# Optimization experiments

Hardware: AMD Instinct MI355X
Metric: run time of the kernel (lower is better)

## Reference

```python
import jax, jax.numpy as jnp
import numpy as np

TOP_K = 8
ROUTED_SCALING_FACTOR = 1.0
EPS = 1e-20


def setup_inputs() -> dict:
    key = jax.random.key(0)
    k1, k2, k3 = jax.random.split(key, 3)
    T, D, E = 8192, 4096, 64
    x = jax.random.normal(k1, (T, D), dtype=jnp.float32)
    gate_weight = jax.random.normal(k2, (E, D), dtype=jnp.float32) * (1.0 / np.sqrt(D))
    bias = jax.random.normal(k3, (E,), dtype=jnp.float32) * 0.1
    return {"x": x, "gate_weight": gate_weight, "bias": bias}


def reference(x, gate_weight, bias):
    # logits: [T, E] = x [T, D] @ gate_weight.T [D, E]
    logits = jnp.einsum('td,ed->te', x.astype(jnp.float32), gate_weight)
    scores = jax.nn.sigmoid(logits)
    biased = scores + bias  # broadcast [E]
    # top-k on biased scores, sorted descending
    _, indices = jax.lax.top_k(biased, TOP_K)  # [T, K]
    selected_scores = jnp.take_along_axis(scores, indices, axis=-1)  # [T, K]
    normalized = selected_scores / (jnp.sum(selected_scores, axis=-1, keepdims=True) + EPS)
    weights = normalized * ROUTED_SCALING_FACTOR
    return (indices, weights)
```

## Files before the change

kernel.cpp:

```cpp
#include <hip/hip_runtime.h>
#include <math.h>
#include <stdint.h>

#define T_TOK 8192
#define DDIM  4096
#define NEXP  64
#define TOPK  8
#define MT    128
#define BK    32
#define RS    2048.0f

typedef __attribute__((ext_vector_type(8))) _Float16 half8;
typedef __attribute__((ext_vector_type(4))) float f32x4;
typedef __attribute__((address_space(3))) uint32_t lds_u32;
typedef const __attribute__((address_space(1))) uint32_t glb_u32;

template<int STEPS, int S>
__global__ __launch_bounds__(512) void gemm_part(
    const float* __restrict__ x, const float* __restrict__ gw,
    float* __restrict__ part)
{
    __shared__ float A[2][MT * BK];
    __shared__ float Bf[2][2048];

    const int tid  = threadIdx.x;
    const int lane = tid & 63;
    const int wv   = tid >> 6;
    const int wm   = wv & 3;
    const int wn   = wv >> 2;
    const int slc  = blockIdx.x % S;
    const int mt   = blockIdx.x / S;
    const int m0   = mt * MT;
    const int kt0  = slc * STEPS;
    const int am   = lane & 15;
    const int ag   = lane >> 4;

    const int s_row0 = tid >> 3;
    const int s_c    = tid & 7;

    const int bn = wv & 3;
    const int bh = wv >> 2;
    const float* gB = gw + (size_t)(bn * 16 + am) * DDIM
                    + (size_t)kt0 * BK + ag * 8 + bh * 4;

#define STAGE(buf_, t_) do {                                                   \
        const size_t koff = (size_t)(kt0 + (t_)) * BK;                         \
        int c0 = s_c ^ (s_row0 & 7);                                           \
        __builtin_amdgcn_global_load_lds(                                      \
            (glb_u32*)(x + (size_t)(m0 + s_row0) * DDIM + koff + c0 * 4),      \
            (lds_u32*)(&A[buf_][tid * 4]), 16, 0, 0);                          \
        int r1 = s_row0 + 64;                                                  \
        int c1 = s_c ^ (r1 & 7);                                               \
        __builtin_amdgcn_global_load_lds(                                      \
            (glb_u32*)(x + (size_t)(m0 + r1) * DDIM + koff + c1 * 4),          \
            (lds_u32*)(&A[buf_][2048 + tid * 4]), 16, 0, 0);                   \
        __builtin_amdgcn_global_load_lds(                                      \
            (glb_u32*)(gB + (size_t)(t_) * BK),                                \
            (lds_u32*)(&Bf[buf_][((bn * 2 + bh) * 64 + lane) * 4]), 16, 0, 0); \
    } while (0)

    f32x4 aH[2][2], aM[2][2];
    #pragma unroll
    for (int f = 0; f < 2; f++)
        #pragma unroll
        for (int n = 0; n < 2; n++) {
            aH[f][n] = (f32x4){0.f, 0.f, 0.f, 0.f};
            aM[f][n] = (f32x4){0.f, 0.f, 0.f, 0.f};
        }

    STAGE(0, 0);
    __syncthreads();

    #pragma unroll 2
    for (int t = 0; t < STEPS; t++) {
        const int buf = t & 1;
        if (t + 1 < STEPS) STAGE(buf ^ 1, t + 1);

        half8 B0[2], B1[2];
        #pragma unroll
        for (int nf = 0; nf < 2; nf++) {
            const int n = wn * 2 + nf;
            float4 u0 = *reinterpret_cast<const float4*>(
                &Bf[buf][((n * 2 + 0) * 64 + lane) * 4]);
            float4 u1 = *reinterpret_cast<const float4*>(
                &Bf[buf][((n * 2 + 1) * 64 + lane) * 4]);
            const float bv[8] = {u0.x, u0.y, u0.z, u0.w, u1.x, u1.y, u1.z, u1.w};
            #pragma unroll
            for (int j = 0; j < 8; j++) {
                float v = bv[j];
                _Float16 h = (_Float16)v;
                B0[nf][j] = h;
                B1[nf][j] = (_Float16)((v - (float)h) * RS);
            }
        }

        #pragma unroll
        for (int f = 0; f < 2; f++) {
            const int row = wm * 32 + f * 16 + am;
            const int sw  = am & 7;
            float4 alo = *reinterpret_cast<const float4*>(
                &A[buf][row * BK + ((ag * 2 + 0) ^ sw) * 4]);
            float4 ahi = *reinterpret_cast<const float4*>(
                &A[buf][row * BK + ((ag * 2 + 1) ^ sw) * 4]);
            const float vv[8] = {alo.x, alo.y, alo.z, alo.w,
                                 ahi.x, ahi.y, ahi.z, ahi.w};
            half8 a0, a1;
            #pragma unroll
            for (int j = 0; j < 8; j++) {
                float v = vv[j];
                _Float16 h = (_Float16)v;
                a0[j] = h;
                a1[j] = (_Float16)((v - (float)h) * RS);
            }
            #pragma unroll
            for (int nf = 0; nf < 2; nf++) {
                aH[f][nf] = __builtin_amdgcn_mfma_f32_16x16x32_f16(a0, B0[nf], aH[f][nf], 0, 0, 0);
                aM[f][nf] = __builtin_amdgcn_mfma_f32_16x16x32_f16(a0, B1[nf], aM[f][nf], 0, 0, 0);
                aM[f][nf] = __builtin_amdgcn_mfma_f32_16x16x32_f16(a1, B0[nf], aM[f][nf], 0, 0, 0);
            }
        }
        __syncthreads();
    }
#undef STAGE

    const float i1 = 1.0f / RS;
    float* po = part + (size_t)slc * T_TOK * NEXP + (size_t)m0 * NEXP;
    #pragma unroll
    for (int f = 0; f < 2; f++)
        #pragma unroll
        for (int nf = 0; nf < 2; nf++)
            #pragma unroll
            for (int r = 0; r < 4; r++)
                po[(size_t)(wm * 32 + f * 16 + ag * 4 + r) * NEXP
                   + (wn * 2 + nf) * 16 + am]
                    = aH[f][nf][r] + aM[f][nf][r] * i1;
}

__global__ __launch_bounds__(256) void reduce_topk(
    const float* __restrict__ part, const float* __restrict__ bias,
    float* __restrict__ out, int S)
{
    const int wave = threadIdx.x >> 6;
    const int lane = threadIdx.x & 63;
    const int j    = blockIdx.x;
    const int g    = j & 7;
    const int q    = j >> 3;
    const int token = g * 128 + (q & 31) * 4 + (q >> 5) * 1024 + wave;
    if (token >= T_TOK) return;

    float logit = 0.f;
    for (int s = 0; s < S; s++)
        logit += part[(size_t)s * T_TOK * NEXP + (size_t)token * NEXP + lane];

    float score  = 1.f / (1.f + expf(-logit));
    float biased = score + bias[lane];

    float my_sc = 0.f;
    int   my_idx = 0;
    float ssum  = 0.f;

    #pragma unroll
    for (int jj = 0; jj < TOPK; jj++) {
        float v = biased;
        int   i = lane;
        #pragma unroll
        for (int off = 32; off >= 1; off >>= 1) {
            float ov = __shfl_xor(v, off);
            int   oi = __shfl_xor(i, off);
            if (ov > v || (ov == v && oi < i)) { v = ov; i = oi; }
        }
        float s_sel = __shfl(score, i);
        ssum += s_sel;
        if (lane == jj) { my_idx = i; my_sc = s_sel; }
        if (lane == i) biased = -INFINITY;
    }

    if (lane < TOPK) {
        out[(size_t)token * TOPK + lane] = (float)my_idx;
        out[(size_t)T_TOK * TOPK + (size_t)token * TOPK + lane]
            = my_sc / (ssum + 1e-20f);
    }
}

extern "C" void kernel_launch(void* const* d_in, const int* in_sizes, int n_in,
                              void* d_out, int out_size, void* d_ws, size_t ws_size,
                              hipStream_t stream) {
    (void)in_sizes; (void)n_in; (void)out_size;
    const float* x    = (const float*)d_in[0];
    const float* gw   = (const float*)d_in[1];
    const float* bias = (const float*)d_in[2];
    float* out  = (float*)d_out;
    float* part = (float*)d_ws;

    const size_t per_slice = (size_t)T_TOK * NEXP * sizeof(float);
    int S = 1;
    for (int cand : {8, 4, 2}) {
        if ((size_t)cand * per_slice <= ws_size) { S = cand; break; }
    }

    dim3 b1(512);
    switch (S) {
        case 8: gemm_part<16, 8><<<dim3(64 * 8), b1, 0, stream>>>(x, gw, part); break;
        case 4: gemm_part<32, 4><<<dim3(64 * 4), b1, 0, stream>>>(x, gw, part); break;
        case 2: gemm_part<64, 2><<<dim3(64 * 2), b1, 0, stream>>>(x, gw, part); break;
        default: gemm_part<128, 1><<<dim3(64), b1, 0, stream>>>(x, gw, part); break;
    }

    reduce_topk<<<dim3(T_TOK / 4), 256, 0, stream>>>(part, bias, out, S);
}
```

Measured before the change: 45.90 us.

## Add 256-row M tile GEMM variant with 16-way split-K

Adds a GEMM kernel with 256-token tiles where each of 8 waves covers 32 rows and all 64 experts. Each wave converts the B (gate weight) fragments to split-fp16 once and reuses them across both of its row fragments. The split-K factor also rises to 16 when the workspace allows, keeping 512 blocks. This is meant to cut redundant B loads and conversions per token, but it doubles the partial-sum traffic the reduce kernel must read and adds register pressure from the larger accumulator set.

```diff
diff --git a/kernel.cpp b/kernel.cpp
--- a/kernel.cpp
+++ b/kernel.cpp
@@ -6,7 +6,6 @@
 #define DDIM  4096
 #define NEXP  64
 #define TOPK  8
-#define MT    128
 #define BK    32
 #define RS    2048.0f
 
@@ -16,11 +15,126 @@
 typedef const __attribute__((address_space(1))) uint32_t glb_u32;
 
 template<int STEPS, int S>
-__global__ __launch_bounds__(512) void gemm_part(
+__global__ __launch_bounds__(512, 4) void gemm_part256(
     const float* __restrict__ x, const float* __restrict__ gw,
     float* __restrict__ part)
 {
-    __shared__ float A[2][MT * BK];
+    __shared__ float A[2][256 * BK];
+    __shared__ float Bf[2][2048];
+
+    const int tid  = threadIdx.x;
+    const int lane = tid & 63;
+    const int wv   = tid >> 6;
+    const int slc  = blockIdx.x % S;
+    const int mt   = blockIdx.x / S;
+    const int m0   = mt * 256;
+    const int kt0  = slc * STEPS;
+    const int am   = lane & 15;
+    const int ag   = lane >> 4;
+
+    const int bn = wv & 3;
+    const int bh = wv >> 2;
+    const float* gB = gw + (size_t)(bn * 16 + am) * DDIM
+                    + (size_t)kt0 * BK + ag * 8 + bh * 4;
+
+#define STAGE(buf_, t_) do {                                                   \
+        const size_t koff = (size_t)(kt0 + (t_)) * BK;                         \
+        _Pragma("unroll")                                                      \
+        for (int r_ = 0; r_ < 4; r_++) {                                       \
+            int idx_ = r_ * 512 + tid;                                         \
+            int row_ = idx_ >> 3;                                              \
+            int c_   = idx_ & 7;                                               \
+            int cs_  = c_ ^ (row_ & 7);                                        \
+            __builtin_amdgcn_global_load_lds(                                  \
+                (glb_u32*)(x + (size_t)(m0 + row_) * DDIM + koff + cs_ * 4),   \
+                (lds_u32*)(&A[buf_][idx_ * 4]), 16, 0, 0);                     \
+        }                                                                      \
+        __builtin_amdgcn_global_load_lds(                                      \
+            (glb_u32*)(gB + (size_t)(t_) * BK),                                \
+            (lds_u32*)(&Bf[buf_][((bn * 2 + bh) * 64 + lane) * 4]), 16, 0, 0); \
+    } while (0)
+
+    f32x4 aH[2][4], aM[2][4];
+    #pragma unroll
+    for (int f = 0; f < 2; f++)
+        #pragma unroll
+        for (int n = 0; n < 4; n++) {
+            aH[f][n] = (f32x4){0.f, 0.f, 0.f, 0.f};
+            aM[f][n] = (f32x4){0.f, 0.f, 0.f, 0.f};
+        }
+
+    STAGE(0, 0);
+    __syncthreads();
+
+    for (int t = 0; t < STEPS; t++) {
+        const int buf = t & 1;
+        if (t + 1 < STEPS) STAGE(buf ^ 1, t + 1);
+
+        half8 a0[2], a1[2];
+        #pragma unroll
+        for (int f = 0; f < 2; f++) {
+            const int row = wv * 32 + f * 16 + am;
+            const int sw  = am & 7;
+            float4 alo = *reinterpret_cast<const float4*>(
+                &A[buf][row * BK + ((ag * 2 + 0) ^ sw) * 4]);
+            float4 ahi = *reinterpret_cast<const float4*>(
+                &A[buf][row * BK + ((ag * 2 + 1) ^ sw) * 4]);
+            const float vv[8] = {alo.x, alo.y, alo.z, alo.w,
+                                 ahi.x, ahi.y, ahi.z, ahi.w};
+            #pragma unroll
+            for (int j = 0; j < 8; j++) {
+                float v = vv[j];
+                _Float16 h = (_Float16)v;
+                a0[f][j] = h;
+                a1[f][j] = (_Float16)((v - (float)h) * RS);
+            }
+        }
+
+        #pragma unroll
+        for (int nf = 0; nf < 4; nf++) {
+            float4 u0 = *reinterpret_cast<const float4*>(
+                &Bf[buf][((nf * 2 + 0) * 64 + lane) * 4]);
+            float4 u1 = *reinterpret_cast<const float4*>(
+                &Bf[buf][((nf * 2 + 1) * 64 + lane) * 4]);
+            const float bv[8] = {u0.x, u0.y, u0.z, u0.w, u1.x, u1.y, u1.z, u1.w};
+            half8 B0, B1;
+            #pragma unroll
+            for (int j = 0; j < 8; j++) {
+                float v = bv[j];
+                _Float16 h = (_Float16)v;
+                B0[j] = h;
+                B1[j] = (_Float16)((v - (float)h) * RS);
+            }
+            #pragma unroll
+            for (int f = 0; f < 2; f++) {
+                aH[f][nf] = __builtin_amdgcn_mfma_f32_16x16x32_f16(a0[f], B0, aH[f][nf], 0, 0, 0);
+                aM[f][nf] = __builtin_amdgcn_mfma_f32_16x16x32_f16(a0[f], B1, aM[f][nf], 0, 0, 0);
+                aM[f][nf] = __builtin_amdgcn_mfma_f32_16x16x32_f16(a1[f], B0, aM[f][nf], 0, 0, 0);
+            }
+        }
+        __syncthreads();
+    }
+#undef STAGE
+
+    const float i1 = 1.0f / RS;
+    float* po = part + (size_t)slc * T_TOK * NEXP + (size_t)m0 * NEXP;
+    #pragma unroll
+    for (int f = 0; f < 2; f++)
+        #pragma unroll
+        for (int nf = 0; nf < 4; nf++)
+            #pragma unroll
+            for (int r = 0; r < 4; r++)
+                po[(size_t)(wv * 32 + f * 16 + ag * 4 + r) * NEXP
+                   + nf * 16 + am]
+                    = aH[f][nf][r] + aM[f][nf][r] * i1;
+}
+
+template<int STEPS, int S>
+__global__ __launch_bounds__(512) void gemm_part128(
+    const float* __restrict__ x, const float* __restrict__ gw,
+    float* __restrict__ part)
+{
+    __shared__ float A[2][128 * BK];
     __shared__ float Bf[2][2048];
 
     const int tid  = threadIdx.x;
@@ -30,7 +144,7 @@
     const int wn   = wv >> 2;
     const int slc  = blockIdx.x % S;
     const int mt   = blockIdx.x / S;
-    const int m0   = mt * MT;
+    const int m0   = mt * 128;
     const int kt0  = slc * STEPS;
     const int am   = lane & 15;
     const int ag   = lane >> 4;
@@ -93,7 +207,6 @@
                 B1[nf][j] = (_Float16)((v - (float)h) * RS);
             }
         }
-
         #pragma unroll
         for (int f = 0; f < 2; f++) {
             const int row = wm * 32 + f * 16 + am;
@@ -194,16 +307,17 @@
 
     const size_t per_slice = (size_t)T_TOK * NEXP * sizeof(float);
     int S = 1;
-    for (int cand : {8, 4, 2}) {
+    for (int cand : {16, 8, 4, 2}) {
         if ((size_t)cand * per_slice <= ws_size) { S = cand; break; }
     }
 
     dim3 b1(512);
     switch (S) {
-        case 8: gemm_part<16, 8><<<dim3(64 * 8), b1, 0, stream>>>(x, gw, part); break;
-        case 4: gemm_part<32, 4><<<dim3(64 * 4), b1, 0, stream>>>(x, gw, part); break;
-        case 2: gemm_part<64, 2><<<dim3(64 * 2), b1, 0, stream>>>(x, gw, part); break;
-        default: gemm_part<128, 1><<<dim3(64), b1, 0, stream>>>(x, gw, part); break;
+        case 16: gemm_part256< 8, 16><<<dim3(32 * 16), b1, 0, stream>>>(x, gw, part); break;
+        case  8: gemm_part128<16,  8><<<dim3(64 *  8), b1, 0, stream>>>(x, gw, part); break;
+        case  4: gemm_part128<32,  4><<<dim3(64 *  4), b1, 0, stream>>>(x, gw, part); break;
+        case  2: gemm_part128<64,  2><<<dim3(64 *  2), b1, 0, stream>>>(x, gw, part); break;
+        default: gemm_part128<128, 1><<<dim3(64), b1, 0, stream>>>(x, gw, part); break;
     }
 
     reduce_topk<<<dim3(T_TOK / 4), 256, 0, stream>>>(part, bias, out, S);
```

New measurement: 48.57 us. +5.8%, slower.
